# Optimization experiments

Hardware: AMD Instinct MI355X
Metric: run time of the kernel (lower is better)

## Reference

```python
import jax, jax.numpy as jnp
import numpy as np

HIDDEN = 512
NUM_HEADS = 8


def setup_inputs() -> dict:
    key = jax.random.key(0)
    ks = jax.random.split(key, 8)
    Tq, Tk, Cq, Ck, H = 1, 65536, 512, 512, HIDDEN
    s = 1.0 / np.sqrt(H)
    return {
        "Q": jax.random.normal(ks[0], (Tq, Cq), jnp.float32),
        "K": jax.random.normal(ks[1], (Tk, Ck), jnp.float32),
        "Wq": jax.random.normal(ks[2], (H, Cq), jnp.float32) * s,
        "bq": jax.random.normal(ks[3], (H,), jnp.float32) * s,
        "Wk": jax.random.normal(ks[4], (H, Ck), jnp.float32) * s,
        "bk": jax.random.normal(ks[5], (H,), jnp.float32) * s,
        "Wout": jax.random.normal(ks[6], (1, NUM_HEADS), jnp.float32) * 0.3,
        "bout": jax.random.normal(ks[7], (1,), jnp.float32) * 0.3,
    }


def reference(Q, K, Wq, bq, Wk, bk, Wout, bout):
    h = NUM_HEADS
    H = Wq.shape[0]
    d = H // h  # per-head dim
    # linear + ReLU projections
    Ql = jax.nn.relu(Q @ Wq.T + bq)          # [1, H]
    Kl = jax.nn.relu(K @ Wk.T + bk)          # [Tk, H]
    # split into heads (T_q == 1 is required by linear_out)
    Qh = Ql.reshape(h, d)                    # [h, d]
    Kh = Kl.reshape(-1, h, d)                # [Tk, h, d]
    # per-head scores, scaled by sqrt(d_head); dropout rate 0 -> identity
    scores = jnp.einsum('hd,thd->th', Qh, Kh) / (d ** 0.5)  # [Tk, h]
    # learned per-head fusion, then softmax over the T_k axis
    logits = scores @ Wout.T + bout          # [Tk, 1]
    return jax.nn.softmax(logits, axis=0)    # [Tk, 1]
```

## Files before the change

### kernel.cpp

```cpp
#include <hip/hip_runtime.h>
#include <hip/hip_fp16.h>

#define CDIM 512
#define ROWS 65536
#define TPW  16

typedef _Float16 half8  __attribute__((ext_vector_type(8)));
typedef __fp16   fp16x2 __attribute__((ext_vector_type(2)));
typedef float    f32x16 __attribute__((ext_vector_type(16)));

__device__ __forceinline__ half8 cvt8(float4 f0, float4 f1) {
    union { fp16x2 h2[4]; half8 h8; } u;
    u.h2[0] = __builtin_amdgcn_cvt_pkrtz(f0.x, f0.y);
    u.h2[1] = __builtin_amdgcn_cvt_pkrtz(f0.z, f0.w);
    u.h2[2] = __builtin_amdgcn_cvt_pkrtz(f1.x, f1.y);
    u.h2[3] = __builtin_amdgcn_cvt_pkrtz(f1.z, f1.w);
    return u.h8;
}

__global__ void prep_kernel(const float* __restrict__ Q, const float* __restrict__ Wq,
                            const float* __restrict__ bq, const float* __restrict__ Wout,
                            const float* __restrict__ Wk,
                            float* __restrict__ v, _Float16* __restrict__ Wkf) {
    __shared__ float qs[CDIM];
    const int t = threadIdx.x;
    if (blockIdx.x < 32) {
        qs[t] = Q[t]; qs[t + 256] = Q[t + 256];
        __syncthreads();
        const int jj  = t >> 4;
        const int sub = t & 15;
        const int j   = blockIdx.x * 16 + jj;
        const float4* w4 = (const float4*)(Wq + (size_t)j * CDIM + sub * 32);
        const float4* q4 = (const float4*)(qs + sub * 32);
        float s = 0.f;
        #pragma unroll
        for (int i = 0; i < 8; ++i) {
            float4 w = w4[i]; float4 q = q4[i];
            s = fmaf(w.x, q.x, s); s = fmaf(w.y, q.y, s);
            s = fmaf(w.z, q.z, s); s = fmaf(w.w, q.w, s);
        }
        s += __shfl_xor(s, 1); s += __shfl_xor(s, 2);
        s += __shfl_xor(s, 4); s += __shfl_xor(s, 8);
        if (sub == 0) {
            s += bq[j];
            s = fmaxf(s, 0.f);
            v[j] = s * Wout[j >> 6] * 0.125f;
        }
    } else {
        const int gid = (blockIdx.x - 32) * 256 + t;
        const int jb  = gid >> 11;
        const int kc  = (gid >> 6) & 31;
        const int l   = gid & 63;
        const int j   = jb * 32 + (l & 31);
        const int k   = kc * 16 + (l >> 5) * 8;
        const float* src = Wk + (size_t)j * CDIM + k;
        float4 f0 = *(const float4*)(src);
        float4 f1 = *(const float4*)(src + 4);
        *(half8*)(Wkf + (size_t)gid * 8) = cvt8(f0, f1);
    }
}

__global__ __launch_bounds__(256, 1) void score_kernel(
    const float* __restrict__ Kmat, const _Float16* __restrict__ Wkf,
    const float* __restrict__ bk, const float* __restrict__ v,
    float* __restrict__ partial2)
{
    __shared__ alignas(16) char fragbuf[2][32768];
    __shared__ float scratch2[2][4][32];

    const int tid  = threadIdx.x;
    const int lane = tid & 63;
    const int wave = tid >> 6;
    const int l31  = lane & 31;
    const int lhi  = lane >> 5;

    const int bid      = blockIdx.x;
    const int cls      = (bid >> 3) & 1;
    const int rowblock = (bid & 7) * 16 + (bid >> 4);
    const int rowbase  = rowblock * (TPW * 32);
    float* pbase = partial2 + (size_t)cls * ROWS;

    half8 B0[32], B1[32];
    {
        const half8* b0 = (const half8*)Wkf + (size_t)(cls * 8 + wave) * 2048 + lane;
        const half8* b1 = (const half8*)Wkf + (size_t)(cls * 8 + 4 + wave) * 2048 + lane;
        #pragma unroll
        for (int kc = 0; kc < 32; ++kc) { B0[kc] = b0[kc * 64]; B1[kc] = b1[kc * 64]; }
    }
    const int j0 = (cls * 8 + wave) * 32 + l31;
    const int j1 = (cls * 8 + 4 + wave) * 32 + l31;
    const float bj0 = bk[j0], vj0 = v[j0];
    const float bj1 = bk[j1], vj1 = v[j1];

    const int srow = lane & 31;
    const int skof = (lane >> 5) * 8;
    const float* gbase = Kmat + (size_t)(rowbase + srow) * CDIM + skof;

    #pragma unroll
    for (int i = 0; i < 8; ++i) {
        const int kc = (i >> 1) * 8 + (i & 1) * 4 + wave;
        float4 f0 = *(const float4*)(gbase + kc * 16);
        float4 f1 = *(const float4*)(gbase + kc * 16 + 4);
        *(half8*)(&fragbuf[0][kc * 1024 + lane * 16]) = cvt8(f0, f1);
    }
    float4 L[8][2];
    #pragma unroll
    for (int i = 0; i < 8; ++i) {
        const int kc = (i >> 1) * 8 + (i & 1) * 4 + wave;
        L[i][0] = *(const float4*)(gbase + 32 * CDIM + kc * 16);
        L[i][1] = *(const float4*)(gbase + 32 * CDIM + kc * 16 + 4);
    }
    __syncthreads();

    for (int t = 0; t < TPW; ++t) {
        const int cur = t & 1;
        const char* sb = fragbuf[cur];
        char* db = fragbuf[cur ^ 1];

        if (t > 0 && tid < 32) {
            const int pt = (t - 1) & 1;
            float s = scratch2[pt][0][tid] + scratch2[pt][1][tid]
                    + scratch2[pt][2][tid] + scratch2[pt][3][tid];
            pbase[rowbase + (t - 1) * 32 + tid] = s;
        }

        f32x16 acc0, acc1;
        #pragma unroll
        for (int r = 0; r < 16; ++r) { acc0[r] = 0.f; acc1[r] = 0.f; }

        #pragma unroll
        for (int kc = 0; kc < 32; kc += 2) {
            half8 a0 = *(const half8*)(sb + kc * 1024 + lane * 16);
            half8 a1 = *(const half8*)(sb + (kc + 1) * 1024 + lane * 16);
            acc0 = __builtin_amdgcn_mfma_f32_32x32x16_f16(a0, B0[kc], acc0, 0, 0, 0);
            acc1 = __builtin_amdgcn_mfma_f32_32x32x16_f16(a0, B1[kc], acc1, 0, 0, 0);
            acc0 = __builtin_amdgcn_mfma_f32_32x32x16_f16(a1, B0[kc + 1], acc0, 0, 0, 0);
            acc1 = __builtin_amdgcn_mfma_f32_32x32x16_f16(a1, B1[kc + 1], acc1, 0, 0, 0);
        }
        __builtin_amdgcn_sched_barrier(0);

        if (t + 1 < TPW) {
            #pragma unroll
            for (int i = 0; i < 8; ++i) {
                const int kc = (i >> 1) * 8 + (i & 1) * 4 + wave;
                *(half8*)(db + kc * 1024 + lane * 16) = cvt8(L[i][0], L[i][1]);
            }
        }
        if (t + 2 < TPW) {
            const float* gt = gbase + (size_t)(t + 2) * 32 * CDIM;
            #pragma unroll
            for (int i = 0; i < 8; ++i) {
                const int kc = (i >> 1) * 8 + (i & 1) * 4 + wave;
                L[i][0] = *(const float4*)(gt + kc * 16);
                L[i][1] = *(const float4*)(gt + kc * 16 + 4);
            }
        }
        __builtin_amdgcn_sched_barrier(0);

        {
            float part[16];
            #pragma unroll
            for (int r = 0; r < 16; ++r)
                part[r] = fmaxf(acc0[r] + bj0, 0.f) * vj0 + fmaxf(acc1[r] + bj1, 0.f) * vj1;

            float q0[8];
            #pragma unroll
            for (int i = 0; i < 8; ++i) {
                const bool b = lane & 1;
                float keep = b ? part[i + 8] : part[i];
                float send = b ? part[i] : part[i + 8];
                q0[i] = keep + __shfl_xor(send, 1);
            }
            float q1[4];
            #pragma unroll
            for (int i = 0; i < 4; ++i) {
                const bool b = lane & 2;
                float keep = b ? q0[i + 4] : q0[i];
                float send = b ? q0[i] : q0[i + 4];
                q1[i] = keep + __shfl_xor(send, 2);
            }
            float q2[2];
            #pragma unroll
            for (int i = 0; i < 2; ++i) {
                const bool b = lane & 4;
                float keep = b ? q1[i + 2] : q1[i];
                float send = b ? q1[i] : q1[i + 2];
                q2[i] = keep + __shfl_xor(send, 4);
            }
            float q3;
            {
                const bool b = lane & 8;
                float keep = b ? q2[1] : q2[0];
                float send = b ? q2[0] : q2[1];
                q3 = keep + __shfl_xor(send, 8);
            }
            float s = q3 + __shfl_xor(q3, 16);
            if (l31 < 16) {
                const int rr  = ((l31 & 1) << 3) | ((l31 & 2) << 1) | ((l31 & 4) >> 1) | ((l31 & 8) >> 3);
                const int row = (rr & 3) + 8 * (rr >> 2) + 4 * lhi;
                scratch2[cur][wave][row] = s;
            }
        }

        __syncthreads();
    }

    if (tid < 32) {
        const int pt = (TPW - 1) & 1;
        float s = scratch2[pt][0][tid] + scratch2[pt][1][tid]
                + scratch2[pt][2][tid] + scratch2[pt][3][tid];
        pbase[rowbase + (TPW - 1) * 32 + tid] = s;
    }
}

__global__ void expsum_kernel(const float* __restrict__ partial2, float* __restrict__ logits,
                              float* __restrict__ blocksum) {
    __shared__ float red[256];
    const int t = threadIdx.x;
    const int row = blockIdx.x * 256 + t;
    const float lg = partial2[row] + partial2[ROWS + row];
    logits[row] = lg;
    red[t] = expf(lg);
    __syncthreads();
    for (int s = 128; s > 0; s >>= 1) {
        if (t < s) red[t] += red[t + s];
        __syncthreads();
    }
    if (t == 0) blocksum[blockIdx.x] = red[0];
}

__global__ void norm_kernel(const float* __restrict__ logits, const float* __restrict__ blocksum,
                            float* __restrict__ out) {
    __shared__ float red[256];
    const int t = threadIdx.x;
    red[t] = blocksum[t];
    __syncthreads();
    for (int s = 128; s > 0; s >>= 1) {
        if (t < s) red[t] += red[t + s];
        __syncthreads();
    }
    const float zinv = 1.0f / red[0];
    const int i = blockIdx.x * 256 + t;
    out[i] = expf(logits[i]) * zinv;
}

extern "C" void kernel_launch(void* const* d_in, const int* in_sizes, int n_in,
                              void* d_out, int out_size, void* d_ws, size_t ws_size,
                              hipStream_t stream) {
    const float* Q    = (const float*)d_in[0];
    const float* Kmat = (const float*)d_in[1];
    const float* Wq   = (const float*)d_in[2];
    const float* bq   = (const float*)d_in[3];
    const float* Wk   = (const float*)d_in[4];
    const float* bk   = (const float*)d_in[5];
    const float* Wout = (const float*)d_in[6];
    float* out = (float*)d_out;

    char* ws = (char*)d_ws;
    _Float16* Wkf   = (_Float16*)(ws);
    float* v        = (float*)(ws + 524288);
    float* partial2 = (float*)(ws + 526336);
    float* logits   = (float*)(ws + 1050624);
    float* blocksum = (float*)(ws + 1312768);

    hipLaunchKernelGGL(prep_kernel,   dim3(160),  dim3(256), 0, stream, Q, Wq, bq, Wout, Wk, v, Wkf);
    hipLaunchKernelGGL(score_kernel,  dim3(256),  dim3(256), 0, stream, Kmat, Wkf, bk, v, partial2);
    hipLaunchKernelGGL(expsum_kernel, dim3(256),  dim3(256), 0, stream, partial2, logits, blocksum);
    hipLaunchKernelGGL(norm_kernel,   dim3(256),  dim3(256), 0, stream, logits, blocksum, out);
}
```

Baseline: 72.77 us.

## Keep K tile in registers and stream Wk chunks through LDS via async loads

```diff
diff --git a/kernel.cpp b/kernel.cpp
--- a/kernel.cpp
+++ b/kernel.cpp
@@ -3,11 +3,14 @@
 
 #define CDIM 512
 #define ROWS 65536
-#define TPW  16
 
 typedef _Float16 half8  __attribute__((ext_vector_type(8)));
 typedef __fp16   fp16x2 __attribute__((ext_vector_type(2)));
 typedef float    f32x16 __attribute__((ext_vector_type(16)));
+
+#define GLD_LDS16(gp, lp) __builtin_amdgcn_global_load_lds( \
+    (const __attribute__((address_space(1))) unsigned int*)(gp), \
+    (__attribute__((address_space(3))) unsigned int*)(lp), 16, 0, 0)
 
 __device__ __forceinline__ half8 cvt8(float4 f0, float4 f1) {
     union { fp16x2 h2[4]; half8 h8; } u;
@@ -60,167 +63,119 @@
     }
 }
 
-__global__ __launch_bounds__(256, 1) void score_kernel(
+__global__ __launch_bounds__(512, 1) void score_kernel(
     const float* __restrict__ Kmat, const _Float16* __restrict__ Wkf,
     const float* __restrict__ bk, const float* __restrict__ v,
-    float* __restrict__ partial2)
+    float* __restrict__ logits)
 {
-    __shared__ alignas(16) char fragbuf[2][32768];
-    __shared__ float scratch2[2][4][32];
+    __shared__ alignas(16) char Bb[2][65536];
 
     const int tid  = threadIdx.x;
     const int lane = tid & 63;
     const int wave = tid >> 6;
     const int l31  = lane & 31;
     const int lhi  = lane >> 5;
-
-    const int bid      = blockIdx.x;
-    const int cls      = (bid >> 3) & 1;
-    const int rowblock = (bid & 7) * 16 + (bid >> 4);
-    const int rowbase  = rowblock * (TPW * 32);
-    float* pbase = partial2 + (size_t)cls * ROWS;
-
-    half8 B0[32], B1[32];
+    const int rowbase = blockIdx.x * 256;
+
+    #pragma unroll
+    for (int i = 0; i < 8; ++i)
+        GLD_LDS16((const char*)Wkf + i * 8192 + tid * 16, Bb[0] + i * 8192 + tid * 16);
+
+    half8 a[32];
     {
-        const half8* b0 = (const half8*)Wkf + (size_t)(cls * 8 + wave) * 2048 + lane;
-        const half8* b1 = (const half8*)Wkf + (size_t)(cls * 8 + 4 + wave) * 2048 + lane;
-        #pragma unroll
-        for (int kc = 0; kc < 32; ++kc) { B0[kc] = b0[kc * 64]; B1[kc] = b1[kc * 64]; }
-    }
-    const int j0 = (cls * 8 + wave) * 32 + l31;
-    const int j1 = (cls * 8 + 4 + wave) * 32 + l31;
-    const float bj0 = bk[j0], vj0 = v[j0];
-    const float bj1 = bk[j1], vj1 = v[j1];
-
-    const int srow = lane & 31;
-    const int skof = (lane >> 5) * 8;
-    const float* gbase = Kmat + (size_t)(rowbase + srow) * CDIM + skof;
-
+        const float* ab = Kmat + (size_t)(rowbase + wave * 32 + l31) * CDIM + lhi * 8;
+        #pragma unroll
+        for (int kc = 0; kc < 32; ++kc) {
+            float4 f0 = *(const float4*)(ab + kc * 16);
+            float4 f1 = *(const float4*)(ab + kc * 16 + 4);
+            a[kc] = cvt8(f0, f1);
+        }
+    }
+
+    float part[16];
     #pragma unroll
-    for (int i = 0; i < 8; ++i) {
-        const int kc = (i >> 1) * 8 + (i & 1) * 4 + wave;
-        float4 f0 = *(const float4*)(gbase + kc * 16);
-        float4 f1 = *(const float4*)(gbase + kc * 16 + 4);
-        *(half8*)(&fragbuf[0][kc * 1024 + lane * 16]) = cvt8(f0, f1);
-    }
-    float4 L[8][2];
-    #pragma unroll
-    for (int i = 0; i < 8; ++i) {
-        const int kc = (i >> 1) * 8 + (i & 1) * 4 + wave;
-        L[i][0] = *(const float4*)(gbase + 32 * CDIM + kc * 16);
-        L[i][1] = *(const float4*)(gbase + 32 * CDIM + kc * 16 + 4);
-    }
+    for (int r = 0; r < 16; ++r) part[r] = 0.f;
+
     __syncthreads();
 
-    for (int t = 0; t < TPW; ++t) {
-        const int cur = t & 1;
-        const char* sb = fragbuf[cur];
-        char* db = fragbuf[cur ^ 1];
-
-        if (t > 0 && tid < 32) {
-            const int pt = (t - 1) & 1;
-            float s = scratch2[pt][0][tid] + scratch2[pt][1][tid]
-                    + scratch2[pt][2][tid] + scratch2[pt][3][tid];
-            pbase[rowbase + (t - 1) * 32 + tid] = s;
-        }
+    for (int c = 0; c < 8; ++c) {
+        const int cur = c & 1;
+
+        if (c < 7) {
+            const char* src = (const char*)Wkf + (size_t)(c + 1) * 65536;
+            #pragma unroll
+            for (int i = 0; i < 8; ++i)
+                GLD_LDS16(src + i * 8192 + tid * 16, Bb[cur ^ 1] + i * 8192 + tid * 16);
+        }
+
+        const int jg0 = c * 64 + l31;
+        const float bj0 = bk[jg0],      vj0 = v[jg0];
+        const float bj1 = bk[jg0 + 32], vj1 = v[jg0 + 32];
 
         f32x16 acc0, acc1;
         #pragma unroll
         for (int r = 0; r < 16; ++r) { acc0[r] = 0.f; acc1[r] = 0.f; }
 
         #pragma unroll
-        for (int kc = 0; kc < 32; kc += 2) {
-            half8 a0 = *(const half8*)(sb + kc * 1024 + lane * 16);
-            half8 a1 = *(const half8*)(sb + (kc + 1) * 1024 + lane * 16);
-            acc0 = __builtin_amdgcn_mfma_f32_32x32x16_f16(a0, B0[kc], acc0, 0, 0, 0);
-            acc1 = __builtin_amdgcn_mfma_f32_32x32x16_f16(a0, B1[kc], acc1, 0, 0, 0);
-            acc0 = __builtin_amdgcn_mfma_f32_32x32x16_f16(a1, B0[kc + 1], acc0, 0, 0, 0);
-            acc1 = __builtin_amdgcn_mfma_f32_32x32x16_f16(a1, B1[kc + 1], acc1, 0, 0, 0);
-        }
-        __builtin_amdgcn_sched_barrier(0);
-
-        if (t + 1 < TPW) {
-            #pragma unroll
-            for (int i = 0; i < 8; ++i) {
-                const int kc = (i >> 1) * 8 + (i & 1) * 4 + wave;
-                *(half8*)(db + kc * 1024 + lane * 16) = cvt8(L[i][0], L[i][1]);
-            }
-        }
-        if (t + 2 < TPW) {
-            const float* gt = gbase + (size_t)(t + 2) * 32 * CDIM;
-            #pragma unroll
-            for (int i = 0; i < 8; ++i) {
-                const int kc = (i >> 1) * 8 + (i & 1) * 4 + wave;
-                L[i][0] = *(const float4*)(gt + kc * 16);
-                L[i][1] = *(const float4*)(gt + kc * 16 + 4);
-            }
-        }
-        __builtin_amdgcn_sched_barrier(0);
-
+        for (int kc = 0; kc < 32; ++kc) {
+            half8 b0 = *(const half8*)(Bb[cur] + kc * 1024 + lane * 16);
+            half8 b1 = *(const half8*)(Bb[cur] + (32 + kc) * 1024 + lane * 16);
+            acc0 = __builtin_amdgcn_mfma_f32_32x32x16_f16(a[kc], b0, acc0, 0, 0, 0);
+            acc1 = __builtin_amdgcn_mfma_f32_32x32x16_f16(a[kc], b1, acc1, 0, 0, 0);
+        }
+
+        #pragma unroll
+        for (int r = 0; r < 16; ++r)
+            part[r] += fmaxf(acc0[r] + bj0, 0.f) * vj0 + fmaxf(acc1[r] + bj1, 0.f) * vj1;
+
+        __syncthreads();
+    }
+
+    {
+        float q0[8];
+        #pragma unroll
+        for (int i = 0; i < 8; ++i) {
+            const bool b = lane & 1;
+            float keep = b ? part[i + 8] : part[i];
+            float send = b ? part[i] : part[i + 8];
+            q0[i] = keep + __shfl_xor(send, 1);
+        }
+        float q1[4];
+        #pragma unroll
+        for (int i = 0; i < 4; ++i) {
+            const bool b = lane & 2;
+            float keep = b ? q0[i + 4] : q0[i];
+            float send = b ? q0[i] : q0[i + 4];
+            q1[i] = keep + __shfl_xor(send, 2);
+        }
+        float q2[2];
+        #pragma unroll
+        for (int i = 0; i < 2; ++i) {
+            const bool b = lane & 4;
+            float keep = b ? q1[i + 2] : q1[i];
+            float send = b ? q1[i] : q1[i + 2];
+            q2[i] = keep + __shfl_xor(send, 4);
+        }
+        float q3;
         {
-            float part[16];
-            #pragma unroll
-            for (int r = 0; r < 16; ++r)
-                part[r] = fmaxf(acc0[r] + bj0, 0.f) * vj0 + fmaxf(acc1[r] + bj1, 0.f) * vj1;
-
-            float q0[8];
-            #pragma unroll
-            for (int i = 0; i < 8; ++i) {
-                const bool b = lane & 1;
-                float keep = b ? part[i + 8] : part[i];
-                float send = b ? part[i] : part[i + 8];
-                q0[i] = keep + __shfl_xor(send, 1);
-            }
-            float q1[4];
-            #pragma unroll
-            for (int i = 0; i < 4; ++i) {
-                const bool b = lane & 2;
-                float keep = b ? q0[i + 4] : q0[i];
-                float send = b ? q0[i] : q0[i + 4];
-                q1[i] = keep + __shfl_xor(send, 2);
-            }
-            float q2[2];
-            #pragma unroll
-            for (int i = 0; i < 2; ++i) {
-                const bool b = lane & 4;
-                float keep = b ? q1[i + 2] : q1[i];
-                float send = b ? q1[i] : q1[i + 2];
-                q2[i] = keep + __shfl_xor(send, 4);
-            }
-            float q3;
-            {
-                const bool b = lane & 8;
-                float keep = b ? q2[1] : q2[0];
-                float send = b ? q2[0] : q2[1];
-                q3 = keep + __shfl_xor(send, 8);
-            }
-            float s = q3 + __shfl_xor(q3, 16);
-            if (l31 < 16) {
-                const int rr  = ((l31 & 1) << 3) | ((l31 & 2) << 1) | ((l31 & 4) >> 1) | ((l31 & 8) >> 3);
-                const int row = (rr & 3) + 8 * (rr >> 2) + 4 * lhi;
-                scratch2[cur][wave][row] = s;
-            }
-        }
-
-        __syncthreads();
-    }
-
-    if (tid < 32) {
-        const int pt = (TPW - 1) & 1;
-        float s = scratch2[pt][0][tid] + scratch2[pt][1][tid]
-                + scratch2[pt][2][tid] + scratch2[pt][3][tid];
-        pbase[rowbase + (TPW - 1) * 32 + tid] = s;
-    }
-}
-
-__global__ void expsum_kernel(const float* __restrict__ partial2, float* __restrict__ logits,
-                              float* __restrict__ blocksum) {
+            const bool b = lane & 8;
+            float keep = b ? q2[1] : q2[0];
+            float send = b ? q2[0] : q2[1];
+            q3 = keep + __shfl_xor(send, 8);
+        }
+        float s = q3 + __shfl_xor(q3, 16);
+        if (l31 < 16) {
+            const int rr  = ((l31 & 1) << 3) | ((l31 & 2) << 1) | ((l31 & 4) >> 1) | ((l31 & 8) >> 3);
+            const int row = (rr & 3) + 8 * (rr >> 2) + 4 * lhi;
+            logits[rowbase + wave * 32 + row] = s;
+        }
+    }
+}
+
+__global__ void expsum_kernel(const float* __restrict__ logits, float* __restrict__ blocksum) {
     __shared__ float red[256];
     const int t = threadIdx.x;
-    const int row = blockIdx.x * 256 + t;
-    const float lg = partial2[row] + partial2[ROWS + row];
-    logits[row] = lg;
-    red[t] = expf(lg);
+    red[t] = expf(logits[blockIdx.x * 256 + t]);
     __syncthreads();
     for (int s = 128; s > 0; s >>= 1) {
         if (t < s) red[t] += red[t + s];
@@ -259,12 +214,11 @@
     char* ws = (char*)d_ws;
     _Float16* Wkf   = (_Float16*)(ws);
     float* v        = (float*)(ws + 524288);
-    float* partial2 = (float*)(ws + 526336);
-    float* logits   = (float*)(ws + 1050624);
-    float* blocksum = (float*)(ws + 1312768);
+    float* logits   = (float*)(ws + 526336);
+    float* blocksum = (float*)(ws + 788480);
 
     hipLaunchKernelGGL(prep_kernel,   dim3(160),  dim3(256), 0, stream, Q, Wq, bq, Wout, Wk, v, Wkf);
-    hipLaunchKernelGGL(score_kernel,  dim3(256),  dim3(256), 0, stream, Kmat, Wkf, bk, v, partial2);
-    hipLaunchKernelGGL(expsum_kernel, dim3(256),  dim3(256), 0, stream, partial2, logits, blocksum);
+    hipLaunchKernelGGL(score_kernel,  dim3(256),  dim3(512), 0, stream, Kmat, Wkf, bk, v, logits);
+    hipLaunchKernelGGL(expsum_kernel, dim3(256),  dim3(256), 0, stream, logits, blocksum);
     hipLaunchKernelGGL(norm_kernel,   dim3(256),  dim3(256), 0, stream, logits, blocksum, out);
 }
```

Result: faster. 62.43 us (-14.2%).
